# Performance work log

Measured on AMD Instinct MI355X. Metric: run time of the kernel, lower is better.

## Reference

```python
import jax, jax.numpy as jnp
import numpy as np
import math


def setup_inputs() -> dict:
    key = jax.random.key(0)
    ks = jax.random.split(key, 6)
    B, L, D, H, R = 4, 2048, 512, 8, 4  # batch, seq, feature_dim, n_heads, n_hashes
    hd = D // H
    x = jax.random.normal(ks[0], (B, L, D), jnp.float32)
    Wqk = jax.random.normal(ks[1], (D, 2 * D), jnp.float32) * 0.02
    bqk = jnp.zeros((2 * D,), jnp.float32)
    Wv = jax.random.normal(ks[2], (D, D), jnp.float32) * 0.02
    bv = jnp.zeros((D,), jnp.float32)
    Wo = jax.random.normal(ks[3], (D, D), jnp.float32) * 0.02
    bo = jnp.zeros((D,), jnp.float32)
    rotations = jax.random.normal(ks[4], (H, R, hd), jnp.float32) * 0.02  # registered buffer
    return {"x": x, "Wqk": Wqk, "bqk": bqk, "Wv": Wv, "bv": bv,
            "Wo": Wo, "bo": bo, "rotations": rotations}


def reference(x, Wqk, bqk, Wv, bv, Wo, bo, rotations):
    B, L, D = x.shape
    H = rotations.shape[0]
    hd = D // H

    qk = x @ Wqk + bqk                      # [B, L, 2D]
    q, k = jnp.split(qk, 2, axis=-1)
    v = x @ Wv + bv                         # [B, L, D]

    def heads(t):  # [B, L, D] -> [B, H, L, hd]
        return t.reshape(B, L, H, hd).transpose(0, 2, 1, 3)

    q, k, v = heads(q), heads(k), heads(v)

    # LSH hashing of Q: random rotations then argmax over [rot, -rot]
    rotated = jnp.einsum('bhld,hrd->bhlr', q, rotations)           # [B, H, L, R]
    buckets = jnp.argmax(jnp.concatenate([rotated, -rotated], axis=-1), axis=-1)  # [B, H, L]

    # bucket-sort gather along sequence
    idx = jnp.argsort(buckets, axis=-1)                            # [B, H, L]
    gather = lambda t: jnp.take_along_axis(t, idx[..., None], axis=2)
    sq, sk, sv = gather(q), gather(k), gather(v)

    # full attention over the bucket-sorted sequence (as in the source)
    dots = jnp.einsum('bhid,bhjd->bhij', sq, sk) / math.sqrt(hd)   # [B, H, L, L]
    attn = jax.nn.softmax(dots, axis=-1)
    out = jnp.einsum('bhij,bhjd->bhid', attn, sv)                  # [B, H, L, hd]

    # restore original sequence order
    restore = jnp.argsort(idx, axis=-1)
    out = jnp.take_along_axis(out, restore[..., None], axis=2)
    out = out.transpose(0, 2, 1, 3).reshape(B, L, D)
    return out @ Wo + bo
```

## Files before the change

### kernel.cpp

```cpp
#include <hip/hip_runtime.h>
#include <hip/hip_bf16.h>
#include <math.h>


typedef __attribute__((ext_vector_type(8))) short bf16x8;
typedef __attribute__((ext_vector_type(4))) float f32x4;

#define LOG2E_8 0.1803368801111244f

__device__ __forceinline__ ushort f2bf(float f) {
    union { float f; uint u; } v; v.f = f;
    uint r = v.u + 0x7fffu + ((v.u >> 16) & 1u);
    return (ushort)(r >> 16);
}

__device__ __forceinline__ uint pk2bf(float a, float b) {
    union { __hip_bfloat162 h; uint u; } c;
    c.h = __float22bfloat162_rn(make_float2(a, b));
    return c.u;
}

__device__ __forceinline__ float vexp2(float x) {
    float r;
    asm volatile("v_exp_f32 %0, %1\n\ts_nop 0" : "=v"(r) : "v"(x));
    return r;
}

__device__ __forceinline__ uint f2u(float x) {
    union { float f; uint u; } c; c.f = x; return c.u;
}

__device__ __forceinline__ uint pktrunc(float hi, float lo) {
    return __builtin_amdgcn_perm(f2u(hi), f2u(lo), 0x07060302u);
}

__device__ __forceinline__ void gload16(const ushort* g, ushort* l) {
    __builtin_amdgcn_global_load_lds(
        (const __attribute__((address_space(1))) uint*)(g),
        (__attribute__((address_space(3))) uint*)(l), 16, 0, 0);
}

__global__ __launch_bounds__(256) void prep_all(
    const float* __restrict__ x, const float* __restrict__ Wqk,
    const float* __restrict__ Wv, const float* __restrict__ Wo,
    const float* __restrict__ bqk, const float* __restrict__ bv,
    ushort* __restrict__ xb, ushort* __restrict__ Wt,
    ushort* __restrict__ Wot, float* __restrict__ biasqkv)
{
    int t = blockIdx.x * 256 + threadIdx.x;
    const int NX = 8192 * 512 / 4, W1 = 1024 * 512, W2 = 512 * 512;
    if (t < NX) {
        float4 v = ((const float4*)x)[t];
        uint2 o;
        o.x = pk2bf(v.x, v.y);
        o.y = pk2bf(v.z, v.w);
        ((uint2*)xb)[t] = o;
    } else if (t < NX + W1) {
        int u = t - NX; int n = u >> 9, k = u & 511;
        Wt[u] = f2bf(Wqk[(size_t)k * 1024 + n]);
    } else if (t < NX + W1 + W2) {
        int u = t - NX - W1; int n = u >> 9, k = u & 511;
        Wt[W1 + u] = f2bf(Wv[(size_t)k * 512 + n]);
    } else if (t < NX + W1 + 2 * W2) {
        int u = t - NX - W1 - W2; int n = u >> 9, k = u & 511;
        Wot[u] = f2bf(Wo[(size_t)k * 512 + n]);
    } else if (t < NX + W1 + 2 * W2 + 1536) {
        int u = t - NX - W1 - 2 * W2;
        biasqkv[u] = (u < 1024) ? bqk[u] : bv[u - 1024];
    }
}

__global__ __launch_bounds__(256) void mfma_gemm_qkv(
    const ushort* __restrict__ A, const ushort* __restrict__ Bt,
    const float* __restrict__ bias,
    ushort* __restrict__ qkout, ushort* __restrict__ vtout)
{
    __shared__ ushort SA[8192];
    __shared__ ushort SB[8192];

    const int tid = threadIdx.x, lane = tid & 63, wave = tid >> 6;
    const int quad = lane >> 4, l16 = lane & 15;
    const int m0 = blockIdx.y * 128, n0 = blockIdx.x * 128;
    const int sub = lane >> 3, gl = lane & 7;
    const int wm = (wave >> 1) * 64, wn = (wave & 1) * 64;

    const ushort* asrc[4]; const ushort* bsrc[4];
    #pragma unroll
    for (int n = 0; n < 4; ++n) {
        int row = wave * 32 + n * 8 + sub;
        int g = gl ^ (row & 7);
        asrc[n] = A  + (size_t)(m0 + row) * 512 + g * 8;
        bsrc[n] = Bt + (size_t)(n0 + row) * 512 + g * 8;
    }

    f32x4 acc[4][4];
    #pragma unroll
    for (int mi = 0; mi < 4; ++mi)
        #pragma unroll
        for (int nj = 0; nj < 4; ++nj) acc[mi][nj] = (f32x4){0.f, 0.f, 0.f, 0.f};

    for (int k0 = 0; k0 < 512; k0 += 64) {
        __syncthreads();
        #pragma unroll
        for (int n = 0; n < 4; ++n) {
            gload16(asrc[n] + k0, &SA[(wave * 32 + n * 8) * 64]);
            gload16(bsrc[n] + k0, &SB[(wave * 32 + n * 8) * 64]);
        }
        __syncthreads();

        #pragma unroll
        for (int kc = 0; kc < 2; ++kc) {
            bf16x8 af[4], bfr[4];
            #pragma unroll
            for (int mi = 0; mi < 4; ++mi) {
                int row = wm + mi * 16 + l16;
                af[mi] = *(const bf16x8*)&SA[row * 64 + (((kc * 4 + quad) ^ (row & 7)) * 8)];
            }
            #pragma unroll
            for (int nj = 0; nj < 4; ++nj) {
                int row = wn + nj * 16 + l16;
                bfr[nj] = *(const bf16x8*)&SB[row * 64 + (((kc * 4 + quad) ^ (row & 7)) * 8)];
            }
            #pragma unroll
            for (int mi = 0; mi < 4; ++mi)
                #pragma unroll
                for (int nj = 0; nj < 4; ++nj)
                    acc[mi][nj] = __builtin_amdgcn_mfma_f32_16x16x32_bf16(
                        af[mi], bfr[nj], acc[mi][nj], 0, 0, 0);
        }
    }

    float bvv[4];
    #pragma unroll
    for (int nj = 0; nj < 4; ++nj) bvv[nj] = bias[n0 + wn + nj * 16 + l16];

    if (n0 < 1024) {
        const float sc = (n0 < 512) ? LOG2E_8 : 1.0f;
        #pragma unroll
        for (int mi = 0; mi < 4; ++mi)
            #pragma unroll
            for (int nj = 0; nj < 4; ++nj)
                #pragma unroll
                for (int r = 0; r < 4; ++r) {
                    size_t row = m0 + wm + mi * 16 + quad * 4 + r;
                    qkout[row * 1024 + n0 + wn + nj * 16 + l16] =
                        f2bf((acc[mi][nj][r] + bvv[nj]) * sc);
                }
    } else {
        const int bb = m0 >> 11;
        #pragma unroll
        for (int mi = 0; mi < 4; ++mi)
            #pragma unroll
            for (int nj = 0; nj < 4; ++nj) {
                int nv = n0 - 1024 + wn + nj * 16 + l16;
                int hh = nv >> 6, d = nv & 63;
                int lpos = (m0 & 2047) + wm + (mi >> 1) * 32 + (mi & 1) * 4 + quad * 8;
                uint2 st;
                st.x = pk2bf(acc[mi][nj][0] + bvv[nj], acc[mi][nj][1] + bvv[nj]);
                st.y = pk2bf(acc[mi][nj][2] + bvv[nj], acc[mi][nj][3] + bvv[nj]);
                *(uint2*)&vtout[((size_t)(bb * 8 + hh) * 64 + d) * 2048 + lpos] = st;
            }
    }
}

__global__ __launch_bounds__(512, 4) void attn_mfma(
    const ushort* __restrict__ qk, const ushort* __restrict__ vt,
    ushort* __restrict__ aout)
{
    __shared__ ushort LDSU[32768];

    const int tid = threadIdx.x, lane = tid & 63, wave = tid >> 6;
    const int quad = lane >> 4, l16 = lane & 15;
    const int grp = wave >> 2, w4 = wave & 3;
    const int bh = blockIdx.x, b = bh >> 3, h = bh & 7;
    const int qblk = blockIdx.y;
    const int q0 = qblk * 128 + w4 * 32;
    const int sub = lane >> 3, gl = lane & 7;
    const int GK = grp * 16384, GV = GK + 8192;

    bf16x8 qf[2][2];
    #pragma unroll
    for (int g = 0; g < 2; ++g)
        #pragma unroll
        for (int kc = 0; kc < 2; ++kc)
            qf[g][kc] = *(const bf16x8*)&qk[(size_t)(b * 2048 + q0 + g * 16 + l16) * 1024
                                           + h * 64 + kc * 32 + quad * 8];

    bf16x8 ONES;
    #pragma unroll
    for (int i = 0; i < 8; ++i) ONES[i] = (short)0x3F80;

    const int r0 = l16 * 64 + ((quad ^ (l16 & 7)) << 3);
    const int r1 = l16 * 64 + (((4 | quad) ^ (l16 & 7)) << 3);

    const int srow = w4 * 16 + sub;
    const int g0 = gl ^ (srow & 7), g1 = gl ^ ((srow + 8) & 7);
    const ushort* k0p = qk + (size_t)(b * 2048 + grp * 1024 + srow)     * 1024 + 512 + h * 64 + g0 * 8;
    const ushort* k1p = qk + (size_t)(b * 2048 + grp * 1024 + srow + 8) * 1024 + 512 + h * 64 + g1 * 8;
    const ushort* v0p = vt + ((size_t)bh * 64 + srow)     * 2048 + grp * 1024 + g0 * 8;
    const ushort* v1p = vt + ((size_t)bh * 64 + srow + 8) * 2048 + grp * 1024 + g1 * 8;

    f32x4 O[2][4], Lacc[2];
    #pragma unroll
    for (int g = 0; g < 2; ++g) {
        Lacc[g] = (f32x4){0.f, 0.f, 0.f, 0.f};
        #pragma unroll
        for (int nd = 0; nd < 4; ++nd) O[g][nd] = (f32x4){0.f, 0.f, 0.f, 0.f};
    }

    gload16(k0p, &LDSU[GK + w4 * 1024]);
    gload16(k1p, &LDSU[GK + w4 * 1024 + 512]);
    gload16(v0p, &LDSU[GV + w4 * 1024]);
    gload16(v1p, &LDSU[GV + w4 * 1024 + 512]);
    k0p += 65536; k1p += 65536; v0p += 64; v1p += 64;
    __syncthreads();

#define ATILE(B)                                                               \
    {                                                                          \
        gload16(k0p, &LDSU[GK + ((B) ^ 1) * 4096 + w4 * 1024]);                \
        gload16(k1p, &LDSU[GK + ((B) ^ 1) * 4096 + w4 * 1024 + 512]);          \
        gload16(v0p, &LDSU[GV + ((B) ^ 1) * 4096 + w4 * 1024]);                \
        gload16(v1p, &LDSU[GV + ((B) ^ 1) * 4096 + w4 * 1024 + 512]);          \
        k0p += 65536; k1p += 65536; v0p += 64; v1p += 64;                      \
        f32x4 S[2][4];                                                         \
        _Pragma("unroll")                                                      \
        for (int g = 0; g < 2; ++g)                                            \
            _Pragma("unroll")                                                  \
            for (int mik = 0; mik < 4; ++mik)                                  \
                S[g][mik] = (f32x4){0.f, 0.f, 0.f, 0.f};                       \
        _Pragma("unroll")                                                      \
        for (int mik = 0; mik < 4; ++mik) {                                    \
            bf16x8 kf0 = *(const bf16x8*)&LDSU[GK + (B) * 4096 + mik * 1024 + r0]; \
            bf16x8 kf1 = *(const bf16x8*)&LDSU[GK + (B) * 4096 + mik * 1024 + r1]; \
            S[0][mik] = __builtin_amdgcn_mfma_f32_16x16x32_bf16(kf0, qf[0][0], S[0][mik], 0, 0, 0); \
            S[1][mik] = __builtin_amdgcn_mfma_f32_16x16x32_bf16(kf0, qf[1][0], S[1][mik], 0, 0, 0); \
            S[0][mik] = __builtin_amdgcn_mfma_f32_16x16x32_bf16(kf1, qf[0][1], S[0][mik], 0, 0, 0); \
            S[1][mik] = __builtin_amdgcn_mfma_f32_16x16x32_bf16(kf1, qf[1][1], S[1][mik], 0, 0, 0); \
        }                                                                      \
        uint pkk[2][4][2];                                                     \
        _Pragma("unroll")                                                      \
        for (int g = 0; g < 2; ++g)                                            \
            _Pragma("unroll")                                                  \
            for (int mik = 0; mik < 4; ++mik) {                                \
                _Pragma("unroll")                                              \
                for (int r = 0; r < 4; ++r)                                    \
                    S[g][mik][r] = vexp2(S[g][mik][r]);                        \
                pkk[g][mik][0] = pktrunc(S[g][mik][1], S[g][mik][0]);          \
                pkk[g][mik][1] = pktrunc(S[g][mik][3], S[g][mik][2]);          \
            }                                                                  \
        _Pragma("unroll")                                                      \
        for (int c = 0; c < 2; ++c) {                                          \
            union { uint u[4]; bf16x8 v; } a0, a1;                             \
            a0.u[0] = pkk[0][2 * c][0]; a0.u[1] = pkk[0][2 * c][1];            \
            a0.u[2] = pkk[0][2 * c + 1][0]; a0.u[3] = pkk[0][2 * c + 1][1];    \
            a1.u[0] = pkk[1][2 * c][0]; a1.u[1] = pkk[1][2 * c][1];            \
            a1.u[2] = pkk[1][2 * c + 1][0]; a1.u[3] = pkk[1][2 * c + 1][1];    \
            Lacc[0] = __builtin_amdgcn_mfma_f32_16x16x32_bf16(a0.v, ONES, Lacc[0], 0, 0, 0); \
            Lacc[1] = __builtin_amdgcn_mfma_f32_16x16x32_bf16(a1.v, ONES, Lacc[1], 0, 0, 0); \
            _Pragma("unroll")                                                  \
            for (int nd = 0; nd < 4; ++nd) {                                   \
                bf16x8 vb = *(const bf16x8*)&LDSU[GV + (B) * 4096 + nd * 1024 + ((c) ? r1 : r0)]; \
                O[0][nd] = __builtin_amdgcn_mfma_f32_16x16x32_bf16(a0.v, vb, O[0][nd], 0, 0, 0); \
                O[1][nd] = __builtin_amdgcn_mfma_f32_16x16x32_bf16(a1.v, vb, O[1][nd], 0, 0, 0); \
            }                                                                  \
        }                                                                      \
        __syncthreads();                                                       \
    }

    for (int t2 = 0; t2 < 8; ++t2) {
        ATILE(0);
        ATILE(1);
    }
#undef ATILE

    float* XO = (float*)&LDSU[16384];
    float* XL = (float*)&LDSU[0];

    if (grp == 1) {
        #pragma unroll
        for (int g = 0; g < 2; ++g) {
            if (l16 == 0)
                #pragma unroll
                for (int r = 0; r < 4; ++r)
                    XL[w4 * 32 + g * 16 + quad * 4 + r] = Lacc[g][r];
            #pragma unroll
            for (int nd = 0; nd < 4; ++nd)
                #pragma unroll
                for (int r = 0; r < 4; ++r)
                    XO[(w4 * 32 + g * 16 + quad * 4 + r) * 64 + nd * 16 + l16] = O[g][nd][r];
        }
    }
    __syncthreads();
    if (grp == 0) {
        #pragma unroll
        for (int g = 0; g < 2; ++g) {
            float inv[4];
            #pragma unroll
            for (int r = 0; r < 4; ++r)
                inv[r] = 1.f / (Lacc[g][r] + XL[w4 * 32 + g * 16 + quad * 4 + r]);
            #pragma unroll
            for (int nd = 0; nd < 4; ++nd)
                #pragma unroll
                for (int r = 0; r < 4; ++r) {
                    float o1 = XO[(w4 * 32 + g * 16 + quad * 4 + r) * 64 + nd * 16 + l16];
                    size_t row = (size_t)b * 2048 + q0 + g * 16 + quad * 4 + r;
                    aout[row * 512 + h * 64 + nd * 16 + l16] =
                        f2bf((O[g][nd][r] + o1) * inv[r]);
                }
        }
    }
}

__global__ __launch_bounds__(256) void mfma_gemm_out(
    const ushort* __restrict__ A, const ushort* __restrict__ Bt,
    const float* __restrict__ bias, float* __restrict__ Cf)
{
    __shared__ ushort SA[8192];
    __shared__ ushort SB[4096];

    const int tid = threadIdx.x, lane = tid & 63, wave = tid >> 6;
    const int quad = lane >> 4, l16 = lane & 15;
    const int m0 = blockIdx.y * 128, n0 = blockIdx.x * 64;
    const int sub = lane >> 3, gl = lane & 7;

    const ushort* asrc[4]; const ushort* bsrc[2];
    #pragma unroll
    for (int n = 0; n < 4; ++n) {
        int row = wave * 32 + n * 8 + sub;
        int g = gl ^ (row & 7);
        asrc[n] = A + (size_t)(m0 + row) * 512 + g * 8;
    }
    #pragma unroll
    for (int n = 0; n < 2; ++n) {
        int row = wave * 16 + n * 8 + sub;
        int g = gl ^ (row & 7);
        bsrc[n] = Bt + (size_t)(n0 + row) * 512 + g * 8;
    }

    f32x4 acc[2][4];
    #pragma unroll
    for (int mi = 0; mi < 2; ++mi)
        #pragma unroll
        for (int nj = 0; nj < 4; ++nj) acc[mi][nj] = (f32x4){0.f, 0.f, 0.f, 0.f};

    for (int k0 = 0; k0 < 512; k0 += 64) {
        __syncthreads();
        #pragma unroll
        for (int n = 0; n < 4; ++n)
            gload16(asrc[n] + k0, &SA[(wave * 32 + n * 8) * 64]);
        #pragma unroll
        for (int n = 0; n < 2; ++n)
            gload16(bsrc[n] + k0, &SB[(wave * 16 + n * 8) * 64]);
        __syncthreads();

        #pragma unroll
        for (int kc = 0; kc < 2; ++kc) {
            bf16x8 af[2], bfr[4];
            #pragma unroll
            for (int mi = 0; mi < 2; ++mi) {
                int row = wave * 32 + mi * 16 + l16;
                af[mi] = *(const bf16x8*)&SA[row * 64 + (((kc * 4 + quad) ^ (row & 7)) * 8)];
            }
            #pragma unroll
            for (int nj = 0; nj < 4; ++nj) {
                int row = nj * 16 + l16;
                bfr[nj] = *(const bf16x8*)&SB[row * 64 + (((kc * 4 + quad) ^ (row & 7)) * 8)];
            }
            #pragma unroll
            for (int mi = 0; mi < 2; ++mi)
                #pragma unroll
                for (int nj = 0; nj < 4; ++nj)
                    acc[mi][nj] = __builtin_amdgcn_mfma_f32_16x16x32_bf16(
                        af[mi], bfr[nj], acc[mi][nj], 0, 0, 0);
        }
    }

    float bvv[4];
    #pragma unroll
    for (int nj = 0; nj < 4; ++nj) bvv[nj] = bias[n0 + nj * 16 + l16];

    #pragma unroll
    for (int mi = 0; mi < 2; ++mi)
        #pragma unroll
        for (int nj = 0; nj < 4; ++nj)
            #pragma unroll
            for (int r = 0; r < 4; ++r) {
                size_t row = m0 + wave * 32 + mi * 16 + quad * 4 + r;
                Cf[row * 512 + n0 + nj * 16 + l16] = acc[mi][nj][r] + bvv[nj];
            }
}

extern "C" void kernel_launch(void* const* d_in, const int* in_sizes, int n_in,
                              void* d_out, int out_size, void* d_ws, size_t ws_size,
                              hipStream_t stream)
{
    const float* x   = (const float*)d_in[0];
    const float* Wqk = (const float*)d_in[1];
    const float* bqk = (const float*)d_in[2];
    const float* Wv  = (const float*)d_in[3];
    const float* bv  = (const float*)d_in[4];
    const float* Wo  = (const float*)d_in[5];
    const float* bo  = (const float*)d_in[6];
    float* out = (float*)d_out;

    ushort* xb    = (ushort*)d_ws;
    ushort* qkb   = xb + (size_t)8192 * 512;
    ushort* vtb   = qkb + (size_t)8192 * 1024;
    ushort* attnb = vtb + (size_t)32 * 64 * 2048;
    ushort* Wt    = attnb + (size_t)8192 * 512;
    ushort* Wot   = Wt + (size_t)1536 * 512;
    float* biasqkv = (float*)(Wot + (size_t)512 * 512);

    prep_all<<<8199, 256, 0, stream>>>(x, Wqk, Wv, Wo, bqk, bv, xb, Wt, Wot, biasqkv);

    mfma_gemm_qkv<<<dim3(12, 64), 256, 0, stream>>>(xb, Wt, biasqkv, qkb, vtb);

    attn_mfma<<<dim3(32, 16), 512, 0, stream>>>(qkb, vtb, attnb);

    mfma_gemm_out<<<dim3(8, 64), 256, 0, stream>>>(attnb, Wot, bo, out);
}
```

Baseline: 155.0 us.

## Tile weight transpose via LDS, add MFMA priority hints, split attention epilogue

The prep kernel now transposes the weight matrices in 64x64 tiles through shared memory with coalesced float4 reads and packed bf16 writes, replacing the old strided per-element gather, and it launches far fewer blocks. The attention inner loop wraps its MFMA sections in s_setprio to favour matrix issue across waves. The attention epilogue now has both wave groups exchange partial sums and each finalize one half of the rows, instead of one group doing all the writes, using padded LDS rows. This spreads epilogue work and cuts uncoalesced weight reads, at the cost of an extra LDS sync and more complex indexing.

```diff
diff --git a/kernel.cpp b/kernel.cpp
--- a/kernel.cpp
+++ b/kernel.cpp
@@ -47,26 +47,57 @@
     ushort* __restrict__ xb, ushort* __restrict__ Wt,
     ushort* __restrict__ Wot, float* __restrict__ biasqkv)
 {
-    int t = blockIdx.x * 256 + threadIdx.x;
-    const int NX = 8192 * 512 / 4, W1 = 1024 * 512, W2 = 512 * 512;
-    if (t < NX) {
+    __shared__ float LT[64][65];
+    const int tid = threadIdx.x;
+    const int bid = blockIdx.x;
+
+    if (bid < 4096) {
+        int t = bid * 256 + tid;
         float4 v = ((const float4*)x)[t];
         uint2 o;
         o.x = pk2bf(v.x, v.y);
         o.y = pk2bf(v.z, v.w);
         ((uint2*)xb)[t] = o;
-    } else if (t < NX + W1) {
-        int u = t - NX; int n = u >> 9, k = u & 511;
-        Wt[u] = f2bf(Wqk[(size_t)k * 1024 + n]);
-    } else if (t < NX + W1 + W2) {
-        int u = t - NX - W1; int n = u >> 9, k = u & 511;
-        Wt[W1 + u] = f2bf(Wv[(size_t)k * 512 + n]);
-    } else if (t < NX + W1 + 2 * W2) {
-        int u = t - NX - W1 - W2; int n = u >> 9, k = u & 511;
-        Wot[u] = f2bf(Wo[(size_t)k * 512 + n]);
-    } else if (t < NX + W1 + 2 * W2 + 1536) {
-        int u = t - NX - W1 - 2 * W2;
-        biasqkv[u] = (u < 1024) ? bqk[u] : bv[u - 1024];
+        return;
+    }
+    if (bid == 4352) {
+        int u = tid;
+        #pragma unroll
+        for (int i = 0; i < 6; ++i, u += 256)
+            biasqkv[u] = (u < 1024) ? bqk[u] : bv[u - 1024];
+        return;
+    }
+
+    int tt = bid - 4096;
+    const float* src; ushort* dst; int ncols, k0, nb;
+    if (tt < 128) {
+        src = Wqk; ncols = 1024; k0 = (tt >> 4) * 64; nb = (tt & 15) * 64;
+        dst = Wt;
+    } else if (tt < 192) {
+        int u = tt - 128;
+        src = Wv; ncols = 512; k0 = (u >> 3) * 64; nb = (u & 7) * 64;
+        dst = Wt + (size_t)1024 * 512;
+    } else {
+        int u = tt - 192;
+        src = Wo; ncols = 512; k0 = (u >> 3) * 64; nb = (u & 7) * 64;
+        dst = Wot;
+    }
+    const int r = tid >> 4, c4 = (tid & 15) * 4;
+    #pragma unroll
+    for (int i = 0; i < 4; ++i) {
+        int row = i * 16 + r;
+        float4 v = *(const float4*)&src[(size_t)(k0 + row) * ncols + nb + c4];
+        LT[c4 + 0][row] = v.x; LT[c4 + 1][row] = v.y;
+        LT[c4 + 2][row] = v.z; LT[c4 + 3][row] = v.w;
+    }
+    __syncthreads();
+    #pragma unroll
+    for (int i = 0; i < 4; ++i) {
+        int nrow = i * 16 + r;
+        uint2 o;
+        o.x = pk2bf(LT[nrow][c4 + 0], LT[nrow][c4 + 1]);
+        o.y = pk2bf(LT[nrow][c4 + 2], LT[nrow][c4 + 3]);
+        *(uint2*)&dst[(size_t)(nb + nrow) * 512 + k0 + c4] = o;
     }
 }
 
@@ -228,6 +259,7 @@
             _Pragma("unroll")                                                  \
             for (int mik = 0; mik < 4; ++mik)                                  \
                 S[g][mik] = (f32x4){0.f, 0.f, 0.f, 0.f};                       \
+        __builtin_amdgcn_s_setprio(1);                                         \
         _Pragma("unroll")                                                      \
         for (int mik = 0; mik < 4; ++mik) {                                    \
             bf16x8 kf0 = *(const bf16x8*)&LDSU[GK + (B) * 4096 + mik * 1024 + r0]; \
@@ -237,6 +269,7 @@
             S[0][mik] = __builtin_amdgcn_mfma_f32_16x16x32_bf16(kf1, qf[0][1], S[0][mik], 0, 0, 0); \
             S[1][mik] = __builtin_amdgcn_mfma_f32_16x16x32_bf16(kf1, qf[1][1], S[1][mik], 0, 0, 0); \
         }                                                                      \
+        __builtin_amdgcn_s_setprio(0);                                         \
         uint pkk[2][4][2];                                                     \
         _Pragma("unroll")                                                      \
         for (int g = 0; g < 2; ++g)                                            \
@@ -248,6 +281,7 @@
                 pkk[g][mik][0] = pktrunc(S[g][mik][1], S[g][mik][0]);          \
                 pkk[g][mik][1] = pktrunc(S[g][mik][3], S[g][mik][2]);          \
             }                                                                  \
+        __builtin_amdgcn_s_setprio(1);                                         \
         _Pragma("unroll")                                                      \
         for (int c = 0; c < 2; ++c) {                                          \
             union { uint u[4]; bf16x8 v; } a0, a1;                             \
@@ -264,6 +298,7 @@
                 O[1][nd] = __builtin_amdgcn_mfma_f32_16x16x32_bf16(a1.v, vb, O[1][nd], 0, 0, 0); \
             }                                                                  \
         }                                                                      \
+        __builtin_amdgcn_s_setprio(0);                                         \
         __syncthreads();                                                       \
     }
 
@@ -273,41 +308,43 @@
     }
 #undef ATILE
 
-    float* XO = (float*)&LDSU[16384];
-    float* XL = (float*)&LDSU[0];
-
-    if (grp == 1) {
-        #pragma unroll
-        for (int g = 0; g < 2; ++g) {
-            if (l16 == 0)
-                #pragma unroll
-                for (int r = 0; r < 4; ++r)
-                    XL[w4 * 32 + g * 16 + quad * 4 + r] = Lacc[g][r];
-            #pragma unroll
-            for (int nd = 0; nd < 4; ++nd)
-                #pragma unroll
-                for (int r = 0; r < 4; ++r)
-                    XO[(w4 * 32 + g * 16 + quad * 4 + r) * 64 + nd * 16 + l16] = O[g][nd][r];
-        }
+    float* XOx = (float*)LDSU;
+    float* XOy = XOx + 64 * 68;
+    float* XLx = XOy + 64 * 68;
+    float* XLy = XLx + 64;
+
+    {
+        const int ge = grp ^ 1;
+        float* XO = grp ? XOx : XOy;
+        float* XL = grp ? XLx : XLy;
+        if (l16 == 0)
+            #pragma unroll
+            for (int r = 0; r < 4; ++r)
+                XL[w4 * 16 + quad * 4 + r] = Lacc[ge][r];
+        #pragma unroll
+        for (int nd = 0; nd < 4; ++nd)
+            #pragma unroll
+            for (int r = 0; r < 4; ++r)
+                XO[(w4 * 16 + quad * 4 + r) * 68 + nd * 16 + l16] = O[ge][nd][r];
     }
     __syncthreads();
-    if (grp == 0) {
-        #pragma unroll
-        for (int g = 0; g < 2; ++g) {
-            float inv[4];
-            #pragma unroll
-            for (int r = 0; r < 4; ++r)
-                inv[r] = 1.f / (Lacc[g][r] + XL[w4 * 32 + g * 16 + quad * 4 + r]);
-            #pragma unroll
-            for (int nd = 0; nd < 4; ++nd)
-                #pragma unroll
-                for (int r = 0; r < 4; ++r) {
-                    float o1 = XO[(w4 * 32 + g * 16 + quad * 4 + r) * 64 + nd * 16 + l16];
-                    size_t row = (size_t)b * 2048 + q0 + g * 16 + quad * 4 + r;
-                    aout[row * 512 + h * 64 + nd * 16 + l16] =
-                        f2bf((O[g][nd][r] + o1) * inv[r]);
-                }
-        }
+    {
+        const int gk = grp;
+        float* XO = grp ? XOy : XOx;
+        float* XL = grp ? XLy : XLx;
+        float inv[4];
+        #pragma unroll
+        for (int r = 0; r < 4; ++r)
+            inv[r] = 1.f / (Lacc[gk][r] + XL[w4 * 16 + quad * 4 + r]);
+        #pragma unroll
+        for (int nd = 0; nd < 4; ++nd)
+            #pragma unroll
+            for (int r = 0; r < 4; ++r) {
+                float o1 = XO[(w4 * 16 + quad * 4 + r) * 68 + nd * 16 + l16];
+                size_t row = (size_t)b * 2048 + q0 + gk * 16 + quad * 4 + r;
+                aout[row * 512 + h * 64 + nd * 16 + l16] =
+                    f2bf((O[gk][nd][r] + o1) * inv[r]);
+            }
     }
 }
 
@@ -411,7 +448,7 @@
     ushort* Wot   = Wt + (size_t)1536 * 512;
     float* biasqkv = (float*)(Wot + (size_t)512 * 512);
 
-    prep_all<<<8199, 256, 0, stream>>>(x, Wqk, Wv, Wo, bqk, bv, xb, Wt, Wot, biasqkv);
+    prep_all<<<4353, 256, 0, stream>>>(x, Wqk, Wv, Wo, bqk, bv, xb, Wt, Wot, biasqkv);
 
     mfma_gemm_qkv<<<dim3(12, 64), 256, 0, stream>>>(xb, Wt, biasqkv, qkb, vtb);
 
```

Result: slower. 169.7 us (+9.4%).
